# Optimization experiments

Hardware: AMD Instinct MI355X
Metric: run time of the kernel (lower is better)

## Reference

```python
import jax, jax.numpy as jnp
import numpy as np

B, N, K = 4, 8192, 16
FEAT = 512
GRID = 45
M = GRID * GRID


def _p(key, shape, scale=0.05):
    return jax.random.normal(key, shape, dtype=jnp.float32) * scale


def setup_inputs() -> dict:
    key = jax.random.key(0)
    ks = jax.random.split(key, 40)
    inp = {"pts": jax.random.normal(ks[0], (B, N, 3), dtype=jnp.float32)}
    specs = {
        "w1": (64, 12), "b1": (64,), "w2": (64, 64), "b2": (64,), "w3": (64, 64), "b3": (64,),
        "g1a": (64, 64), "g1ab": (64,), "g1b": (128, 64), "g1bb": (128,),
        "g2a": (128, 128), "g2ab": (128,), "g2b": (1024, 128), "g2bb": (1024,),
        "m1": (FEAT, 1024), "m1b": (FEAT,), "m2": (FEAT, FEAT), "m2b": (FEAT,),
        "f1a": (FEAT, FEAT + 2), "f1ab": (FEAT,), "f1b": (FEAT, FEAT), "f1bb": (FEAT,), "f1c": (3, FEAT), "f1cb": (3,),
        "f2a": (FEAT, FEAT + 3), "f2ab": (FEAT,), "f2b": (FEAT, FEAT), "f2bb": (FEAT,), "f2c": (3, FEAT), "f2cb": (3,),
    }
    for i, (name, shp) in enumerate(specs.items()):
        inp[name] = _p(ks[i + 1], shp)
    return inp


def conv1x1(x, w, b):
    # x: (B,C,N), w: (Cout,Cin), b: (Cout,)
    return jnp.einsum('bcn,oc->bon', x, w) + b[None, :, None]


def knn_idx(x, k):
    # x: (B,C,N) -> neighbor indices (B,N,k) by smallest squared distance (self included)
    xt = jnp.swapaxes(x, 1, 2)                      # (B,N,C)
    sq = jnp.sum(xt * xt, axis=-1)                  # (B,N)
    inner = jnp.einsum('bnc,bmc->bnm', xt, xt)      # (B,N,N)
    neg_d2 = 2.0 * inner - sq[:, :, None] - sq[:, None, :]
    return jax.lax.top_k(neg_d2, k)[1]


def gather_nbrs(feats_t, idx):
    # feats_t: (B,N,C), idx: (B,N,k) -> (B,N,k,C)
    return jax.vmap(lambda f, i: f[i])(feats_t, idx)


def local_maxpool(x, idx):
    # x: (B,C,N) -> (B,C,N) max over k neighbors
    nb = gather_nbrs(jnp.swapaxes(x, 1, 2), idx)    # (B,N,k,C)
    return jnp.swapaxes(jnp.max(nb, axis=2), 1, 2)


def local_cov(pts_t, idx):
    # pts_t: (B,3,N) -> (B,12,N): coords + outer product of first two neighbors
    p = jnp.swapaxes(pts_t, 1, 2)                   # (B,N,3)
    nb = gather_nbrs(p, idx)                        # (B,N,k,3)
    outer = nb[:, :, 0, :, None] * nb[:, :, 1, None, :]   # (B,N,3,3)
    feat = jnp.concatenate([p, outer.reshape(p.shape[0], p.shape[1], 9)], axis=-1)
    return jnp.swapaxes(feat, 1, 2)


def _forward(pts, w1, b1, w2, b2, w3, b3, g1a, g1ab, g1b, g1bb, g2a, g2ab, g2b, g2bb,
             m1, m1b, m2, m2b, f1a, f1ab, f1b, f1bb, f1c, f1cb, f2a, f2ab, f2b, f2bb, f2c, f2cb):
    relu = jax.nn.relu
    pts_t = jnp.swapaxes(pts, 1, 2)                 # (B,3,N)
    # ---- encoder ----
    idx = knn_idx(pts_t, K)
    x = local_cov(pts_t, idx)                       # (B,12,N)
    x = relu(conv1x1(x, w1, b1))
    x = relu(conv1x1(x, w2, b2))
    x = relu(conv1x1(x, w3, b3))                    # (B,64,N)
    idx = knn_idx(x, K)
    g = local_maxpool(x, idx)
    g = conv1x1(relu(conv1x1(g, g1a, g1ab)), g1b, g1bb)   # (B,128,N)
    idx = knn_idx(g, K)
    h = local_maxpool(g, idx)
    h = conv1x1(relu(conv1x1(h, g2a, g2ab)), g2b, g2bb)   # (B,1024,N)
    glob = jnp.max(h, axis=2, keepdims=True)        # (B,1024,1)
    code = conv1x1(relu(conv1x1(glob, m1, m1b)), m2, m2b)  # (B,FEAT,1)
    # ---- decoder ----
    Bs = code.shape[0]
    cw = jnp.broadcast_to(code, (Bs, FEAT, M))
    lin = jnp.linspace(-0.3, 0.3, GRID, dtype=jnp.float32)
    gx, gy = jnp.meshgrid(lin, lin, indexing='ij')
    grid = jnp.stack([gx.ravel(), gy.ravel()], axis=0)     # (2,M)
    grid = jnp.broadcast_to(grid[None], (Bs, 2, M))

    def fold(points, wa, ba, wb, bb, wc, bc):
        y = jnp.concatenate([cw, points], axis=1)
        y = relu(conv1x1(y, wa, ba))
        y = relu(conv1x1(y, wb, bb))
        return conv1x1(y, wc, bc)                    # (B,3,M)

    mid = fold(grid, f1a, f1ab, f1b, f1bb, f1c, f1cb)
    rec = fold(mid, f2a, f2ab, f2b, f2bb, f2c, f2cb)
    return jnp.swapaxes(rec, 1, 2)                   # (B,M,3)


def reference(pts, w1, b1, w2, b2, w3, b3, g1a, g1ab, g1b, g1bb, g2a, g2ab, g2b, g2bb,
              m1, m1b, m2, m2b, f1a, f1ab, f1b, f1bb, f1c, f1cb, f2a, f2ab, f2b, f2bb, f2c, f2cb):
    return _forward(pts, w1, b1, w2, b2, w3, b3, g1a, g1ab, g1b, g1bb, g2a, g2ab, g2b, g2bb,
                    m1, m1b, m2, m2b, f1a, f1ab, f1b, f1bb, f1c, f1cb, f2a, f2ab, f2b, f2bb, f2c, f2cb)
```

## Files before the change

kernel.cpp:

```cpp
#include <hip/hip_runtime.h>
#include <stdint.h>

#define B_ 4
#define N_ 8192
#define K_ 16
#define FEAT_ 512
#define GRID_ 45
#define M_ (GRID_*GRID_)

typedef unsigned long long ull;
typedef __bf16 bf16x8 __attribute__((ext_vector_type(8)));
typedef float f32x16 __attribute__((ext_vector_type(16)));


__device__ __forceinline__ unsigned int fmap(float f){
  unsigned int u = __float_as_uint(f);
  return (u & 0x80000000u) ? ~u : (u | 0x80000000u);
}
__device__ __forceinline__ float funmap(unsigned int u){
  return (u & 0x80000000u) ? __uint_as_float(u ^ 0x80000000u) : __uint_as_float(~u);
}

__device__ __forceinline__ void ins16(ull (&d)[16], ull k){
  if (k < d[15]){
    bool c[16];
#pragma unroll
    for (int s = 0; s < 16; ++s) c[s] = k < d[s];
#pragma unroll
    for (int s = 15; s >= 1; --s) d[s] = c[s-1] ? d[s-1] : (c[s] ? k : d[s]);
    if (c[0]) d[0] = k;
  }
}

__device__ __forceinline__ void ins16b(unsigned (&dk)[16], unsigned (&di)[16],
                                       unsigned k, unsigned id){
  if (k < dk[15]){
    bool c[16];
#pragma unroll
    for (int s = 0; s < 16; ++s) c[s] = k < dk[s];
#pragma unroll
    for (int s = 15; s >= 1; --s){
      dk[s] = c[s-1] ? dk[s-1] : (c[s] ? k  : dk[s]);
      di[s] = c[s-1] ? di[s-1] : (c[s] ? id : di[s]);
    }
    if (c[0]){ dk[0] = k; di[0] = id; }
  }
}

#define GLDS16(l, g) __builtin_amdgcn_global_load_lds((const __attribute__((address_space(1))) void*)(g), (__attribute__((address_space(3))) void*)(l), 16, 0, 0)
#define GLDS4(l, g)  __builtin_amdgcn_global_load_lds((const __attribute__((address_space(1))) void*)(g), (__attribute__((address_space(3))) void*)(l), 4, 0, 0)

#define KEY_INF 0xFF800000FFFFFFFFull

__global__ void k_init(unsigned int* glob){
  int i = blockIdx.x*256 + threadIdx.x;
  if (i < B_*1024) glob[i] = 0x007FFFFFu;
}

__global__ __launch_bounds__(256) void k_nn1(const float* __restrict__ pts,
                                             unsigned long long* __restrict__ nn64){
  __shared__ __align__(16) float sp4[2048][4];
  int b = blockIdx.z, s = blockIdx.y;
  int c0 = s*2048;
  const float* P = pts + (size_t)b*N_*3;
  for (int p = threadIdx.x; p < 2048; p += 256){
    const float* src = P + (size_t)(c0 + p)*3;
    sp4[p][0] = src[0]; sp4[p][1] = src[1]; sp4[p][2] = src[2]; sp4[p][3] = 0.f;
  }
  __syncthreads();
  int n = blockIdx.x*256 + threadIdx.x;
  float qx = P[n*3], qy = P[n*3+1], qz = P[n*3+2];
  float best = 1e30f; int bi = 0;
  for (int j = 0; j < 2048; ++j){
    float4 sv = *(const float4*)sp4[j];
    float dx = qx - sv.x, dy = qy - sv.y, dz = qz - sv.z;
    float d2 = fmaf(dx,dx, fmaf(dy,dy, dz*dz));
    int cj = c0 + j;
    if (d2 < best && cj != n){ best = d2; bi = cj; }
  }
  unsigned long long key = ((unsigned long long)__float_as_uint(best) << 32) | (unsigned int)bi;
  atomicMin(&nn64[(size_t)b*N_ + n], key);
}

__global__ __launch_bounds__(256) void k_cov_mlp(const float* __restrict__ pts,
    const unsigned long long* __restrict__ nn64,
    const float* __restrict__ w1, const float* __restrict__ b1,
    const float* __restrict__ w2, const float* __restrict__ b2,
    const float* __restrict__ w3, const float* __restrict__ b3,
    float* __restrict__ xout){
  __shared__ __align__(16) float W1t[12*64];
  __shared__ __align__(16) float W2t[64*64];
  __shared__ __align__(16) float W3t[64*64];
  __shared__ float B1[64], B2[64], B3[64];
  __shared__ __align__(16) float x0[64][12];
  __shared__ __align__(16) float h1[64][64];
  __shared__ __align__(16) float h2[64][64];
  int b = blockIdx.y; int n0 = blockIdx.x*64; int tid = threadIdx.x;
  for (int i = tid; i < 12*64; i += 256){ int o = i % 64, ci = i / 64; W1t[i] = w1[o*12 + ci]; }
  for (int i = tid; i < 64*64; i += 256){ int o = i % 64, ci = i / 64; W2t[i] = w2[o*64 + ci]; W3t[i] = w3[o*64 + ci]; }
  if (tid < 64){ B1[tid]=b1[tid]; B2[tid]=b2[tid]; B3[tid]=b3[tid]; }
  {
    int p = tid % 64, cg = tid / 64;
    int n = n0 + p;
    const float* P = pts + ((size_t)b*N_ + n)*3;
    int nb = (int)(nn64[(size_t)b*N_ + n] & 0xFFFFFFFFull);
    const float* Q = pts + ((size_t)b*N_ + nb)*3;
    if (cg == 0){ x0[p][0]=P[0]; x0[p][1]=P[1]; x0[p][2]=P[2]; }
    else { int i = cg-1; float pi = P[i];
      x0[p][3+i*3+0]=pi*Q[0]; x0[p][3+i*3+1]=pi*Q[1]; x0[p][3+i*3+2]=pi*Q[2]; }
  }
  __syncthreads();
  { int o = tid % 64, pg = tid / 64;
    for (int p = pg; p < 64; p += 4){
      float acc = B1[o];
#pragma unroll
      for (int ci = 0; ci < 12; ++ci) acc = fmaf(W1t[ci*64+o], x0[p][ci], acc);
      h1[p][o] = fmaxf(acc, 0.f);
    } }
  __syncthreads();
  { int o = tid % 64, pg = tid / 64;
    for (int p = pg; p < 64; p += 4){
      float acc = B2[o];
#pragma unroll
      for (int ci = 0; ci < 64; ++ci) acc = fmaf(W2t[ci*64+o], h1[p][ci], acc);
      h2[p][o] = fmaxf(acc, 0.f);
    } }
  __syncthreads();
  { int o = tid % 64, pg = tid / 64;
    for (int p = pg; p < 64; p += 4){
      float acc = B3[o];
#pragma unroll
      for (int ci = 0; ci < 64; ++ci) acc = fmaf(W3t[ci*64+o], h2[p][ci], acc);
      xout[((size_t)b*N_ + n0 + p)*64 + o] = fmaxf(acc, 0.f);
    } }
}

template<int KF>
__global__ __launch_bounds__(256) void k_prep4(const float* __restrict__ f,
    unsigned short* __restrict__ T, float* __restrict__ cc){
  int b = blockIdx.y; int n = blockIdx.x*256 + threadIdx.x;
  const float* src = f + ((size_t)b*N_ + n)*(KF*16);
  char* Tb = (char*)T;
  float ss = 0.f;
#pragma unroll
  for (int kf = 0; kf < KF; ++kf){
    float v[16];
#pragma unroll
    for (int c4 = 0; c4 < 4; ++c4){
      float4 t4 = *(const float4*)&src[kf*16 + c4*4];
      v[c4*4]=t4.x; v[c4*4+1]=t4.y; v[c4*4+2]=t4.z; v[c4*4+3]=t4.w;
    }
    unsigned short hs[16], ls[16];
#pragma unroll
    for (int c = 0; c < 16; ++c){
      float x = v[c];
      ss = fmaf(x, x, ss);
      __bf16 h = (__bf16)x;
      __bf16 l = (__bf16)(x - (float)h);
      hs[c] = __builtin_bit_cast(unsigned short, h);
      ls[c] = __builtin_bit_cast(unsigned short, l);
    }
    size_t base = ((((size_t)b*KF + kf)*2)*2)*(size_t)(N_*16) + (size_t)n*16;
    const size_t HS = (size_t)N_*16;
    const size_t PS = 2*HS;
    *(uint4*)(Tb + base)            = *(uint4*)&hs[0];
    *(uint4*)(Tb + base + HS)       = *(uint4*)&hs[8];
    *(uint4*)(Tb + base + PS)       = *(uint4*)&ls[0];
    *(uint4*)(Tb + base + PS + HS)  = *(uint4*)&ls[8];
  }
  cc[(size_t)b*N_ + n] = ss;
}

template<int KF, int MW, int S>
__global__ __launch_bounds__(256, MW) void k_knnF(const unsigned short* __restrict__ T,
    const float* __restrict__ ccg, ull* __restrict__ qkeys){
  extern __shared__ char smem[];
  constexpr int NT = (N_/S)/64;
  char* As = smem;
  char* Cs = smem + KF*4096;

  const int tid = threadIdx.x, lane = tid & 63, wid = tid >> 6;
  const int hi = lane >> 5, l31 = lane & 31;
  const int b = blockIdx.z, sp = blockIdx.y, q0 = blockIdx.x*128;
  const int c0 = sp*(N_/S);
  const char* Tb = (const char*)T;
  const size_t HS = (size_t)N_*16, PS = 2*HS, KS = 4*HS;
  const size_t Bb = (size_t)b*KF*KS;
  const float* ccb = ccg + (size_t)b*N_;

  const int q = q0 + wid*32 + l31;
  bf16x8 qh[KF], ql[KF];
#pragma unroll
  for (int kf = 0; kf < KF; ++kf){
    size_t o = Bb + kf*KS + hi*HS + (size_t)q*16;
    qh[kf] = *(const bf16x8*)(Tb + o);
    ql[kf] = *(const bf16x8*)(Tb + o + PS);
  }

  unsigned dk[16], di[16];
#pragma unroll
  for (int t = 0; t < 16; ++t){ dk[t] = 0xFFFFFFFFu; di[t] = 0xFFFFFFFFu; }
  float kapf = __builtin_inff();

  auto stage = [&](int t0){
#pragma unroll
    for (int si = 0; si < KF; ++si){
      int s = wid + 4*si;
      int kf = s >> 2, pl = (s >> 1) & 1, h = s & 1;
      GLDS16(As + s*1024,
             Tb + Bb + kf*KS + pl*PS + h*HS + (size_t)(c0 + t0)*16);
    }
    if (wid == 0) GLDS4(Cs, (const char*)(ccb + c0 + t0));
  };

  for (int t = 0; t < NT; ++t){
    const int t0 = t*64;
    __syncthreads();
    stage(t0);
    asm volatile("s_waitcnt vmcnt(0)" ::: "memory");
    __syncthreads();

    const char* Ab = As + hi*1024 + l31*16;
    const float* cct = (const float*)Cs;
#pragma unroll
    for (int i = 0; i < 2; ++i){
      f32x16 acc = (f32x16)(0.f);
#pragma unroll
      for (int kf = 0; kf < KF; ++kf){
        bf16x8 ah = *(const bf16x8*)(Ab + kf*4096 + i*512);
        bf16x8 al = *(const bf16x8*)(Ab + kf*4096 + 2048 + i*512);
        acc = __builtin_amdgcn_mfma_f32_32x32x16_bf16(ah, qh[kf], acc, 0, 0, 0);
        acc = __builtin_amdgcn_mfma_f32_32x32x16_bf16(ah, ql[kf], acc, 0, 0, 0);
        acc = __builtin_amdgcn_mfma_f32_32x32x16_bf16(al, qh[kf], acc, 0, 0, 0);
      }
#pragma unroll
      for (int rq = 0; rq < 4; ++rq){
        float4 c4 = *(const float4*)(cct + i*32 + 4*hi + 8*rq);
        int rowb = c0 + t0 + i*32 + 4*hi + 8*rq;
        float v0 = fmaf(-2.f, acc[rq*4+0], c4.x);
        float v1 = fmaf(-2.f, acc[rq*4+1], c4.y);
        float v2 = fmaf(-2.f, acc[rq*4+2], c4.z);
        float v3 = fmaf(-2.f, acc[rq*4+3], c4.w);
        if (fminf(fminf(v0, v1), fminf(v2, v3)) < kapf){
          if (v0 < kapf) ins16b(dk, di, fmap(v0), (unsigned)(rowb+0));
          if (v1 < kapf) ins16b(dk, di, fmap(v1), (unsigned)(rowb+1));
          if (v2 < kapf) ins16b(dk, di, fmap(v2), (unsigned)(rowb+2));
          if (v3 < kapf) ins16b(dk, di, fmap(v3), (unsigned)(rowb+3));
          unsigned kk = dk[15];
          kapf = (kk >= 0xFF800000u) ? __builtin_inff() : funmap(kk);
        }
      }
    }
  }
  ull* op = qkeys + (((size_t)((size_t)b*N_ + q)*S + sp)*2 + hi)*16;
#pragma unroll
  for (int t = 0; t < 16; ++t) op[t] = ((ull)dk[t] << 32) | di[t];
}

template<int S>
__global__ void k_sel(const ull* __restrict__ qkeys, int* __restrict__ idxout){
  int i = blockIdx.x*256 + threadIdx.x;
  if (i >= B_*N_) return;
  ull best[16];
#pragma unroll
  for (int t = 0; t < 16; ++t) best[t] = KEY_INF;
  const ull* kp = qkeys + (size_t)i*(S*32);
  for (int t = 0; t < S*32; ++t) ins16(best, kp[t]);
  int* op = idxout + (size_t)i*16;
#pragma unroll
  for (int t = 0; t < 16; ++t) op[t] = (int)(best[t] & 0xffffffffu);
}

__global__ __launch_bounds__(256) void k_gpool_mlp(const float* __restrict__ x,
    const int* __restrict__ idx,
    const float* __restrict__ g1a, const float* __restrict__ g1ab,
    const float* __restrict__ g1b, const float* __restrict__ g1bb,
    float* __restrict__ gout){
  __shared__ __align__(16) float Wt1[64*64];
  __shared__ __align__(16) float Wt2[64*128];
  __shared__ float Ba[64], Bb[128];
  __shared__ __align__(16) float m[64][64];
  __shared__ __align__(16) float r[64][64];
  int b = blockIdx.y; int n0 = blockIdx.x*64; int tid = threadIdx.x;
  for (int i = tid; i < 64*64; i += 256){ int o = i%64, ci = i/64; Wt1[i] = g1a[o*64+ci]; }
  for (int i = tid; i < 64*128; i += 256){ int o = i%128, ci = i/128; Wt2[i] = g1b[o*64+ci]; }
  if (tid < 64) Ba[tid] = g1ab[tid];
  if (tid < 128) Bb[tid] = g1bb[tid];
  { int p = tid/4, cg = tid%4; int n = n0 + p;
    const int* ip = idx + ((size_t)b*N_ + n)*16;
    float mm[16];
#pragma unroll
    for (int u = 0; u < 16; ++u) mm[u] = -1e30f;
    for (int k = 0; k < 16; ++k){
      int nb = ip[k];
      const float4* src = (const float4*)(x + ((size_t)b*N_ + nb)*64 + cg*16);
#pragma unroll
      for (int u = 0; u < 4; ++u){
        float4 v = src[u];
        mm[4*u  ] = fmaxf(mm[4*u  ], v.x); mm[4*u+1] = fmaxf(mm[4*u+1], v.y);
        mm[4*u+2] = fmaxf(mm[4*u+2], v.z); mm[4*u+3] = fmaxf(mm[4*u+3], v.w);
      }
    }
#pragma unroll
    for (int u = 0; u < 16; ++u) m[p][cg*16+u] = mm[u];
  }
  __syncthreads();
  { int o = tid%64, pg = tid/64;
    float acc[16];
#pragma unroll
    for (int u = 0; u < 16; ++u) acc[u] = Ba[o];
    for (int ci = 0; ci < 64; ci += 4){
      float w0 = Wt1[ci*64+o], w1_ = Wt1[(ci+1)*64+o], w2_ = Wt1[(ci+2)*64+o], w3_ = Wt1[(ci+3)*64+o];
#pragma unroll
      for (int u = 0; u < 16; ++u){
        float4 mv = *(const float4*)&m[pg*16+u][ci];
        acc[u] = fmaf(w0, mv.x, acc[u]); acc[u] = fmaf(w1_, mv.y, acc[u]);
        acc[u] = fmaf(w2_, mv.z, acc[u]); acc[u] = fmaf(w3_, mv.w, acc[u]);
      }
    }
#pragma unroll
    for (int u = 0; u < 16; ++u) r[pg*16+u][o] = fmaxf(acc[u], 0.f);
  }
  __syncthreads();
  { int o = tid%128, pg = tid/128;
    float acc[32];
#pragma unroll
    for (int u = 0; u < 32; ++u) acc[u] = Bb[o];
    for (int ci = 0; ci < 64; ci += 4){
      float w0 = Wt2[ci*128+o], w1_ = Wt2[(ci+1)*128+o], w2_ = Wt2[(ci+2)*128+o], w3_ = Wt2[(ci+3)*128+o];
#pragma unroll
      for (int u = 0; u < 32; ++u){
        float4 rv = *(const float4*)&r[pg*32+u][ci];
        acc[u] = fmaf(w0, rv.x, acc[u]); acc[u] = fmaf(w1_, rv.y, acc[u]);
        acc[u] = fmaf(w2_, rv.z, acc[u]); acc[u] = fmaf(w3_, rv.w, acc[u]);
      }
    }
#pragma unroll
    for (int u = 0; u < 32; ++u)
      gout[((size_t)b*N_ + n0 + pg*32 + u)*128 + o] = acc[u];
  }
}

__global__ __launch_bounds__(256) void k_hpool_max(const float* __restrict__ g,
    const int* __restrict__ idx,
    const float* __restrict__ g2a, const float* __restrict__ g2ab,
    const float* __restrict__ g2b, const float* __restrict__ g2bb,
    unsigned int* __restrict__ glob){
  __shared__ __align__(16) float m[32][128];
  __shared__ __align__(16) float t[32][128];
  int b = blockIdx.y; int n0 = blockIdx.x*32; int tid = threadIdx.x;
  { int p = tid/8, cg = tid%8; int n = n0+p;
    const int* ip = idx + ((size_t)b*N_+n)*16;
    float mm[16];
#pragma unroll
    for (int u = 0; u < 16; ++u) mm[u] = -1e30f;
    for (int k = 0; k < 16; ++k){
      int nb = ip[k];
      const float4* src = (const float4*)(g + ((size_t)b*N_+nb)*128 + cg*16);
#pragma unroll
      for (int u = 0; u < 4; ++u){
        float4 v = src[u];
        mm[4*u  ] = fmaxf(mm[4*u  ], v.x); mm[4*u+1] = fmaxf(mm[4*u+1], v.y);
        mm[4*u+2] = fmaxf(mm[4*u+2], v.z); mm[4*u+3] = fmaxf(mm[4*u+3], v.w);
      }
    }
#pragma unroll
    for (int u = 0; u < 16; ++u) m[p][cg*16+u] = mm[u];
  }
  __syncthreads();
  { int o = tid%128, pg = tid/128;
    float acc[16];
#pragma unroll
    for (int u = 0; u < 16; ++u) acc[u] = g2ab[o];
    const float4* wrow = (const float4*)(g2a + (size_t)o*128);
    for (int c4 = 0; c4 < 32; ++c4){
      float4 wv = wrow[c4];
#pragma unroll
      for (int u = 0; u < 16; ++u){
        float4 mv = *(const float4*)&m[pg*16+u][c4*4];
        acc[u] = fmaf(wv.x,mv.x,acc[u]); acc[u] = fmaf(wv.y,mv.y,acc[u]);
        acc[u] = fmaf(wv.z,mv.z,acc[u]); acc[u] = fmaf(wv.w,mv.w,acc[u]);
      }
    }
#pragma unroll
    for (int u = 0; u < 16; ++u) t[pg*16+u][o] = fmaxf(acc[u], 0.f);
  }
  __syncthreads();
  for (int oc = 0; oc < 4; ++oc){
    int o = oc*256 + tid;
    const float4* wrow = (const float4*)(g2b + (size_t)o*128);
    float acc[32];
#pragma unroll
    for (int u = 0; u < 32; ++u) acc[u] = 0.f;
    for (int c4 = 0; c4 < 32; ++c4){
      float4 wv = wrow[c4];
#pragma unroll
      for (int u = 0; u < 32; ++u){
        float4 tv = *(const float4*)&t[u][c4*4];
        acc[u] = fmaf(wv.x,tv.x,acc[u]); acc[u] = fmaf(wv.y,tv.y,acc[u]);
        acc[u] = fmaf(wv.z,tv.z,acc[u]); acc[u] = fmaf(wv.w,tv.w,acc[u]);
      }
    }
    float bias = g2bb[o];
    float mx = -1e30f;
#pragma unroll
    for (int u = 0; u < 32; ++u) mx = fmaxf(mx, acc[u] + bias);
    atomicMax(&glob[b*1024 + o], fmap(mx));
  }
}

__global__ __launch_bounds__(512) void k_code(const unsigned int* __restrict__ glob,
    const float* __restrict__ m1, const float* __restrict__ m1b,
    const float* __restrict__ m2, const float* __restrict__ m2b,
    const float* __restrict__ f1a, const float* __restrict__ f1ab,
    const float* __restrict__ f2a, const float* __restrict__ f2ab,
    float* __restrict__ base1, float* __restrict__ base2){
  __shared__ __align__(16) float gl_s[1024];
  __shared__ __align__(16) float hid_s[512];
  __shared__ __align__(16) float code_s[512];
  int b = blockIdx.x; int tid = threadIdx.x;
  for (int i = tid; i < 1024; i += 512) gl_s[i] = funmap(glob[b*1024+i]);
  __syncthreads();
  { float acc = m1b[tid];
    const float4* wr = (const float4*)(m1 + (size_t)tid*1024);
    for (int c4 = 0; c4 < 256; ++c4){ float4 wv = wr[c4]; float4 gv = *(const float4*)&gl_s[c4*4];
      acc = fmaf(wv.x,gv.x,acc); acc = fmaf(wv.y,gv.y,acc);
      acc = fmaf(wv.z,gv.z,acc); acc = fmaf(wv.w,gv.w,acc); }
    hid_s[tid] = fmaxf(acc, 0.f);
  }
  __syncthreads();
  { float acc = m2b[tid];
    const float4* wr = (const float4*)(m2 + (size_t)tid*512);
    for (int c4 = 0; c4 < 128; ++c4){ float4 wv = wr[c4]; float4 hv = *(const float4*)&hid_s[c4*4];
      acc = fmaf(wv.x,hv.x,acc); acc = fmaf(wv.y,hv.y,acc);
      acc = fmaf(wv.z,hv.z,acc); acc = fmaf(wv.w,hv.w,acc); }
    code_s[tid] = acc;
  }
  __syncthreads();
  { float acc = f1ab[tid];
    const float* wr = f1a + (size_t)tid*514;
    for (int c = 0; c < 512; ++c) acc = fmaf(wr[c], code_s[c], acc);
    base1[b*512 + tid] = acc;
  }
  { float acc = f2ab[tid];
    const float* wr = f2a + (size_t)tid*515;
    for (int c = 0; c < 512; ++c) acc = fmaf(wr[c], code_s[c], acc);
    base2[b*512 + tid] = acc;
  }
}

template<int NIN>
__global__ __launch_bounds__(256) void k_fold(const float* __restrict__ base,
    const float* __restrict__ fa,
    const float* __restrict__ fb, const float* __restrict__ fbb,
    const float* __restrict__ fc, const float* __restrict__ fcb,
    const float* __restrict__ pin, float* __restrict__ pout){
  __shared__ __align__(16) float y1[32][512];
  __shared__ __align__(16) float y2[32][516];
  __shared__ float pcoord[32][NIN];
  int b = blockIdx.y; int m0 = blockIdx.x*32; int tid = threadIdx.x;
  if (tid < 32*NIN){
    int p = tid / NIN, c = tid % NIN;
    int mm = min(m0 + p, M_-1);
    float v;
    if (NIN == 2){
      const float step = 0.6f/44.f;
      int ii = (c == 0) ? (mm/GRID_) : (mm%GRID_);
      v = -0.3f + step*ii;
    } else {
      v = pin[((size_t)b*M_ + mm)*3 + c];
    }
    pcoord[p][c] = v;
  }
  __syncthreads();
  const int stride_a = 512 + NIN;
  for (int rep = 0; rep < 2; ++rep){
    int o = rep*256 + tid;
    float av[NIN];
#pragma unroll
    for (int c = 0; c < NIN; ++c) av[c] = fa[(size_t)o*stride_a + 512 + c];
    float bv = base[b*512 + o];
    for (int p = 0; p < 32; ++p){
      float acc = bv;
#pragma unroll
      for (int c = 0; c < NIN; ++c) acc = fmaf(av[c], pcoord[p][c], acc);
      y1[p][o] = fmaxf(acc, 0.f);
    }
  }
  __syncthreads();
  for (int rep = 0; rep < 2; ++rep){
    int o2 = rep*256 + tid;
    const float* wr = fb + (size_t)o2*512;
    float acc[32];
#pragma unroll
    for (int u = 0; u < 32; ++u) acc[u] = 0.f;
    for (int c4 = 0; c4 < 128; ++c4){
      float4 wv = *(const float4*)&wr[c4*4];
#pragma unroll
      for (int u = 0; u < 32; ++u){
        float4 yv = *(const float4*)&y1[u][c4*4];
        acc[u] = fmaf(wv.x,yv.x,acc[u]); acc[u] = fmaf(wv.y,yv.y,acc[u]);
        acc[u] = fmaf(wv.z,yv.z,acc[u]); acc[u] = fmaf(wv.w,yv.w,acc[u]);
      }
    }
    float bias = fbb[o2];
#pragma unroll
    for (int u = 0; u < 32; ++u) y2[u][o2] = fmaxf(acc[u] + bias, 0.f);
  }
  __syncthreads();
  if (tid < 96){
    int p = tid / 3, c = tid % 3;
    const float* wr = fc + (size_t)c*512;
    float acc = fcb[c];
    for (int o4 = 0; o4 < 128; ++o4){
      float4 wv = *(const float4*)&wr[o4*4];
      float4 yv = *(const float4*)&y2[p][o4*4];
      acc = fmaf(wv.x,yv.x,acc); acc = fmaf(wv.y,yv.y,acc);
      acc = fmaf(wv.z,yv.z,acc); acc = fmaf(wv.w,yv.w,acc);
    }
    int mm = m0 + p;
    if (mm < M_) pout[((size_t)b*M_ + mm)*3 + c] = acc;
  }
}

extern "C" void kernel_launch(void* const* d_in, const int* in_sizes, int n_in,
                              void* d_out, int out_size, void* d_ws, size_t ws_size,
                              hipStream_t stream){
  const float* pts  = (const float*)d_in[0];
  const float* w1   = (const float*)d_in[1];  const float* b1   = (const float*)d_in[2];
  const float* w2   = (const float*)d_in[3];  const float* b2   = (const float*)d_in[4];
  const float* w3   = (const float*)d_in[5];  const float* b3   = (const float*)d_in[6];
  const float* g1a  = (const float*)d_in[7];  const float* g1ab = (const float*)d_in[8];
  const float* g1b  = (const float*)d_in[9];  const float* g1bb = (const float*)d_in[10];
  const float* g2a  = (const float*)d_in[11]; const float* g2ab = (const float*)d_in[12];
  const float* g2b  = (const float*)d_in[13]; const float* g2bb = (const float*)d_in[14];
  const float* m1   = (const float*)d_in[15]; const float* m1b  = (const float*)d_in[16];
  const float* m2   = (const float*)d_in[17]; const float* m2b  = (const float*)d_in[18];
  const float* f1a  = (const float*)d_in[19]; const float* f1ab = (const float*)d_in[20];
  const float* f1b  = (const float*)d_in[21]; const float* f1bb = (const float*)d_in[22];
  const float* f1c  = (const float*)d_in[23]; const float* f1cb = (const float*)d_in[24];
  const float* f2a  = (const float*)d_in[25]; const float* f2ab = (const float*)d_in[26];
  const float* f2b  = (const float*)d_in[27]; const float* f2bb = (const float*)d_in[28];
  const float* f2c  = (const float*)d_in[29]; const float* f2cb = (const float*)d_in[30];
  float* out = (float*)d_out;

  char* w = (char*)d_ws;
  auto alloc = [&](size_t bytes){ char* p = w; w += (bytes + 255) & ~(size_t)255; return p; };
  unsigned long long* nn64 = (unsigned long long*)alloc((size_t)B_*N_*8);
  float* x    = (float*)alloc((size_t)B_*N_*64*4);
  float* g    = (float*)alloc((size_t)B_*N_*128*4);
  unsigned short* T64  = (unsigned short*)alloc((size_t)B_*4*4*N_*16);
  unsigned short* T128 = (unsigned short*)alloc((size_t)B_*8*4*N_*16);
  float* ccf  = (float*)alloc((size_t)B_*N_*4);
  int*   idx  = (int*)alloc((size_t)B_*N_*16*4);
  ull*   qkeys = (ull*)alloc((size_t)B_*N_*4*2*16*8);
  unsigned int* glob = (unsigned int*)alloc((size_t)B_*1024*4);
  float* base1 = (float*)alloc((size_t)B_*512*4);
  float* base2 = (float*)alloc((size_t)B_*512*4);
  float* mid   = (float*)alloc((size_t)B_*M_*3*4);
  (void)ws_size; (void)in_sizes; (void)n_in; (void)out_size;

  const int SMEM4 = 4*4096 + 256;
  const int SMEM8 = 8*4096 + 256;
  hipFuncSetAttribute((const void*)k_knnF<4,4,4>, hipFuncAttributeMaxDynamicSharedMemorySize, SMEM4);
  hipFuncSetAttribute((const void*)k_knnF<8,4,4>, hipFuncAttributeMaxDynamicSharedMemorySize, SMEM8);

  hipMemsetAsync(nn64, 0xFF, (size_t)B_*N_*8, stream);
  k_init<<<dim3((B_*1024+255)/256), 256, 0, stream>>>(glob);
  k_nn1<<<dim3(N_/256, 4, B_), 256, 0, stream>>>(pts, nn64);
  k_cov_mlp<<<dim3(N_/64, B_), 256, 0, stream>>>(pts, nn64, w1,b1,w2,b2,w3,b3, x);

  k_prep4<4><<<dim3(N_/256, B_), 256, 0, stream>>>(x, T64, ccf);
  k_knnF<4,4,4><<<dim3(N_/128, 4, B_), 256, SMEM4, stream>>>(T64, ccf, qkeys);
  k_sel<4><<<dim3(B_*N_/256), 256, 0, stream>>>(qkeys, idx);

  k_gpool_mlp<<<dim3(N_/64, B_), 256, 0, stream>>>(x, idx, g1a,g1ab,g1b,g1bb, g);

  k_prep4<8><<<dim3(N_/256, B_), 256, 0, stream>>>(g, T128, ccf);
  k_knnF<8,4,4><<<dim3(N_/128, 4, B_), 256, SMEM8, stream>>>(T128, ccf, qkeys);
  k_sel<4><<<dim3(B_*N_/256), 256, 0, stream>>>(qkeys, idx);

  k_hpool_max<<<dim3(N_/32, B_), 256, 0, stream>>>(g, idx, g2a,g2ab,g2b,g2bb, glob);
  k_code<<<dim3(B_), 512, 0, stream>>>(glob, m1,m1b,m2,m2b, f1a,f1ab, f2a,f2ab, base1, base2);
  k_fold<2><<<dim3((M_+31)/32, B_), 256, 0, stream>>>(base1, f1a, f1b, f1bb, f1c, f1cb, nullptr, mid);
  k_fold<3><<<dim3((M_+31)/32, B_), 256, 0, stream>>>(base2, f2a, f2b, f2bb, f2c, f2cb, mid, out);
}
```

Baseline: 1.781 ms.

## Fuse bf16 split prep into cov MLP, shrink fold tiles, retune knn occupancy

The cov MLP kernel now writes the bf16 hi/lo split tensor and the squared norms directly from shared memory, so the separate prep launch and its reread of x are gone. The fold kernels drop from 32 to 16 points per block, which doubles the block count and halves per-thread accumulators to improve occupancy. The 128-channel knn kernel's launch-bounds occupancy hint changes from 4 to 3. Together these trade less redundant global traffic and better parallelism in small kernels against more weight reloads in the fold GEMMs.

```diff
diff --git a/kernel.cpp b/kernel.cpp
--- a/kernel.cpp
+++ b/kernel.cpp
@@ -45,6 +45,13 @@
     }
     if (c[0]){ dk[0] = k; di[0] = id; }
   }
+}
+
+__device__ __forceinline__ void bsplit(float x, unsigned short& h, unsigned short& l){
+  __bf16 hh = (__bf16)x;
+  __bf16 ll = (__bf16)(x - (float)hh);
+  h = __builtin_bit_cast(unsigned short, hh);
+  l = __builtin_bit_cast(unsigned short, ll);
 }
 
 #define GLDS16(l, g) __builtin_amdgcn_global_load_lds((const __attribute__((address_space(1))) void*)(g), (__attribute__((address_space(3))) void*)(l), 16, 0, 0)
@@ -87,7 +94,8 @@
     const float* __restrict__ w1, const float* __restrict__ b1,
     const float* __restrict__ w2, const float* __restrict__ b2,
     const float* __restrict__ w3, const float* __restrict__ b3,
-    float* __restrict__ xout){
+    float* __restrict__ xout, unsigned short* __restrict__ T,
+    float* __restrict__ cc){
   __shared__ __align__(16) float W1t[12*64];
   __shared__ __align__(16) float W2t[64*64];
   __shared__ __align__(16) float W3t[64*64];
@@ -131,8 +139,32 @@
       float acc = B3[o];
 #pragma unroll
       for (int ci = 0; ci < 64; ++ci) acc = fmaf(W3t[ci*64+o], h2[p][ci], acc);
-      xout[((size_t)b*N_ + n0 + p)*64 + o] = fmaxf(acc, 0.f);
+      float r = fmaxf(acc, 0.f);
+      xout[((size_t)b*N_ + n0 + p)*64 + o] = r;
+      h1[p][o] = r;
     } }
+  __syncthreads();
+  {
+    char* Tb = (char*)T;
+    const size_t HS = (size_t)N_*16, PS = 2*HS, KS = 4*HS;
+    const size_t Bb = (size_t)b*4*KS;
+    for (int e = tid; e < 64*8; e += 256){
+      int p = e >> 3, gg = e & 7;
+      int kf = gg >> 1, h = gg & 1;
+      unsigned short hs[8], ls[8];
+#pragma unroll
+      for (int j = 0; j < 8; ++j) bsplit(h1[p][gg*8+j], hs[j], ls[j]);
+      size_t base = Bb + (size_t)kf*KS + (size_t)h*HS + (size_t)(n0+p)*16;
+      *(uint4*)(Tb + base)      = *(uint4*)hs;
+      *(uint4*)(Tb + base + PS) = *(uint4*)ls;
+    }
+    if (tid < 64){
+      float ss = 0.f;
+#pragma unroll 8
+      for (int c = 0; c < 64; ++c){ float v = h1[tid][(c + tid) & 63]; ss = fmaf(v, v, ss); }
+      cc[(size_t)b*N_ + n0 + tid] = ss;
+    }
+  }
 }
 
 template<int KF>
@@ -155,10 +187,7 @@
     for (int c = 0; c < 16; ++c){
       float x = v[c];
       ss = fmaf(x, x, ss);
-      __bf16 h = (__bf16)x;
-      __bf16 l = (__bf16)(x - (float)h);
-      hs[c] = __builtin_bit_cast(unsigned short, h);
-      ls[c] = __builtin_bit_cast(unsigned short, l);
+      bsplit(x, hs[c], ls[c]);
     }
     size_t base = ((((size_t)b*KF + kf)*2)*2)*(size_t)(N_*16) + (size_t)n*16;
     const size_t HS = (size_t)N_*16;
@@ -455,11 +484,11 @@
     const float* __restrict__ fb, const float* __restrict__ fbb,
     const float* __restrict__ fc, const float* __restrict__ fcb,
     const float* __restrict__ pin, float* __restrict__ pout){
-  __shared__ __align__(16) float y1[32][512];
-  __shared__ __align__(16) float y2[32][516];
-  __shared__ float pcoord[32][NIN];
-  int b = blockIdx.y; int m0 = blockIdx.x*32; int tid = threadIdx.x;
-  if (tid < 32*NIN){
+  __shared__ __align__(16) float y1[16][512];
+  __shared__ __align__(16) float y2[16][516];
+  __shared__ float pcoord[16][NIN];
+  int b = blockIdx.y; int m0 = blockIdx.x*16; int tid = threadIdx.x;
+  if (tid < 16*NIN){
     int p = tid / NIN, c = tid % NIN;
     int mm = min(m0 + p, M_-1);
     float v;
@@ -480,7 +509,8 @@
 #pragma unroll
     for (int c = 0; c < NIN; ++c) av[c] = fa[(size_t)o*stride_a + 512 + c];
     float bv = base[b*512 + o];
-    for (int p = 0; p < 32; ++p){
+#pragma unroll
+    for (int p = 0; p < 16; ++p){
       float acc = bv;
 #pragma unroll
       for (int c = 0; c < NIN; ++c) acc = fmaf(av[c], pcoord[p][c], acc);
@@ -491,13 +521,13 @@
   for (int rep = 0; rep < 2; ++rep){
     int o2 = rep*256 + tid;
     const float* wr = fb + (size_t)o2*512;
-    float acc[32];
-#pragma unroll
-    for (int u = 0; u < 32; ++u) acc[u] = 0.f;
+    float acc[16];
+#pragma unroll
+    for (int u = 0; u < 16; ++u) acc[u] = 0.f;
     for (int c4 = 0; c4 < 128; ++c4){
       float4 wv = *(const float4*)&wr[c4*4];
 #pragma unroll
-      for (int u = 0; u < 32; ++u){
+      for (int u = 0; u < 16; ++u){
         float4 yv = *(const float4*)&y1[u][c4*4];
         acc[u] = fmaf(wv.x,yv.x,acc[u]); acc[u] = fmaf(wv.y,yv.y,acc[u]);
         acc[u] = fmaf(wv.z,yv.z,acc[u]); acc[u] = fmaf(wv.w,yv.w,acc[u]);
@@ -505,10 +535,10 @@
     }
     float bias = fbb[o2];
 #pragma unroll
-    for (int u = 0; u < 32; ++u) y2[u][o2] = fmaxf(acc[u] + bias, 0.f);
-  }
-  __syncthreads();
-  if (tid < 96){
+    for (int u = 0; u < 16; ++u) y2[u][o2] = fmaxf(acc[u] + bias, 0.f);
+  }
+  __syncthreads();
+  if (tid < 48){
     int p = tid / 3, c = tid % 3;
     const float* wr = fc + (size_t)c*512;
     float acc = fcb[c];
@@ -563,25 +593,24 @@
   const int SMEM4 = 4*4096 + 256;
   const int SMEM8 = 8*4096 + 256;
   hipFuncSetAttribute((const void*)k_knnF<4,4,4>, hipFuncAttributeMaxDynamicSharedMemorySize, SMEM4);
-  hipFuncSetAttribute((const void*)k_knnF<8,4,4>, hipFuncAttributeMaxDynamicSharedMemorySize, SMEM8);
+  hipFuncSetAttribute((const void*)k_knnF<8,3,4>, hipFuncAttributeMaxDynamicSharedMemorySize, SMEM8);
 
   hipMemsetAsync(nn64, 0xFF, (size_t)B_*N_*8, stream);
   k_init<<<dim3((B_*1024+255)/256), 256, 0, stream>>>(glob);
   k_nn1<<<dim3(N_/256, 4, B_), 256, 0, stream>>>(pts, nn64);
-  k_cov_mlp<<<dim3(N_/64, B_), 256, 0, stream>>>(pts, nn64, w1,b1,w2,b2,w3,b3, x);
-
-  k_prep4<4><<<dim3(N_/256, B_), 256, 0, stream>>>(x, T64, ccf);
+  k_cov_mlp<<<dim3(N_/64, B_), 256, 0, stream>>>(pts, nn64, w1,b1,w2,b2,w3,b3, x, T64, ccf);
+
   k_knnF<4,4,4><<<dim3(N_/128, 4, B_), 256, SMEM4, stream>>>(T64, ccf, qkeys);
   k_sel<4><<<dim3(B_*N_/256), 256, 0, stream>>>(qkeys, idx);
 
   k_gpool_mlp<<<dim3(N_/64, B_), 256, 0, stream>>>(x, idx, g1a,g1ab,g1b,g1bb, g);
 
   k_prep4<8><<<dim3(N_/256, B_), 256, 0, stream>>>(g, T128, ccf);
-  k_knnF<8,4,4><<<dim3(N_/128, 4, B_), 256, SMEM8, stream>>>(T128, ccf, qkeys);
+  k_knnF<8,3,4><<<dim3(N_/128, 4, B_), 256, SMEM8, stream>>>(T128, ccf, qkeys);
   k_sel<4><<<dim3(B_*N_/256), 256, 0, stream>>>(qkeys, idx);
 
   k_hpool_max<<<dim3(N_/32, B_), 256, 0, stream>>>(g, idx, g2a,g2ab,g2b,g2bb, glob);
   k_code<<<dim3(B_), 512, 0, stream>>>(glob, m1,m1b,m2,m2b, f1a,f1ab, f2a,f2ab, base1, base2);
-  k_fold<2><<<dim3((M_+31)/32, B_), 256, 0, stream>>>(base1, f1a, f1b, f1bb, f1c, f1cb, nullptr, mid);
-  k_fold<3><<<dim3((M_+31)/32, B_), 256, 0, stream>>>(base2, f2a, f2b, f2bb, f2c, f2cb, mid, out);
-}
+  k_fold<2><<<dim3((M_+15)/16, B_), 256, 0, stream>>>(base1, f1a, f1b, f1bb, f1c, f1cb, nullptr, mid);
+  k_fold<3><<<dim3((M_+15)/16, B_), 256, 0, stream>>>(base2, f2a, f2b, f2bb, f2c, f2cb, mid, out);
+}
```

Result: faster. 1.638 ms (-8.0%).
